# Kernel tuning notes

Measured on AMD Instinct MI355X. Metric: run time of the kernel, lower is better.

## Reference

```python
import jax, jax.numpy as jnp
import numpy as np

C = 512        # in_ch = n_heads * d_embed
NH = 8         # heads
DH = C // NH   # head dim = 64
G = 32         # groups
EPS_GN = 1e-6
EPS_LN = 1e-5


def group_norm(x, gamma, beta):
    # x: (B, C, H, W)
    B, Cc, H, W = x.shape
    xg = x.reshape(B, G, Cc // G, H, W)
    mu = xg.mean(axis=(2, 3, 4), keepdims=True)
    var = xg.var(axis=(2, 3, 4), keepdims=True)
    xg = (xg - mu) * jax.lax.rsqrt(var + EPS_GN)
    x = xg.reshape(B, Cc, H, W)
    return x * gamma[None, :, None, None] + beta[None, :, None, None]


def layer_norm(x, gamma, beta):
    mu = x.mean(axis=-1, keepdims=True)
    var = x.var(axis=-1, keepdims=True)
    return (x - mu) * jax.lax.rsqrt(var + EPS_LN) * gamma + beta


def mhsa(x, w_qkv, w_out, b_out):
    # x: (B, S, C); w_qkv: (C, 3C); w_out: (C, C)
    B, S, Cc = x.shape
    qkv = x @ w_qkv                                   # (B, S, 3C)
    q, k, v = jnp.split(qkv, 3, axis=-1)
    q = q.reshape(B, S, NH, DH).transpose(0, 2, 1, 3)  # (B, H, S, D)
    k = k.reshape(B, S, NH, DH).transpose(0, 2, 1, 3)
    v = v.reshape(B, S, NH, DH).transpose(0, 2, 1, 3)
    scores = jnp.einsum('bhsd,bhtd->bhst', q, k) / jnp.sqrt(jnp.float32(DH))
    attn = jax.nn.softmax(scores, axis=-1)
    o = jnp.einsum('bhst,bhtd->bhsd', attn, v)         # (B, H, S, D)
    o = o.transpose(0, 2, 1, 3).reshape(B, S, Cc)
    return o @ w_out + b_out


def conv1x1(x, w, b):
    # x: (B, C, H, W); w: (Cout, Cin)
    return jnp.einsum('oc,bchw->bohw', w, x) + b[None, :, None, None]


def reference(x, gn_g, gn_b, w_cin, b_cin,
              ln1_g, ln1_b, qkv1, out1_w, out1_b,
              ln2_g, ln2_b, qkv2, out2_w, out2_b,
              ln3_g, ln3_b, g1_w, g1_b, g2_w, g2_b,
              w_cout, b_cout):
    residue_long = x
    h = group_norm(x, gn_g, gn_b)
    h = conv1x1(h, w_cin, b_cin)
    B, Cc, H, W = h.shape
    h = h.reshape(B, Cc, H * W).transpose(0, 2, 1)     # (B, S, C)

    r = h
    h = mhsa(layer_norm(h, ln1_g, ln1_b), qkv1, out1_w, out1_b) + r
    r = h
    h = mhsa(layer_norm(h, ln2_g, ln2_b), qkv2, out2_w, out2_b) + r
    r = h
    g = layer_norm(h, ln3_g, ln3_b) @ g1_w + g1_b      # (B, S, 8C)
    val, gate = jnp.split(g, 2, axis=-1)
    h = (val * jax.nn.gelu(gate, approximate=False)) @ g2_w + g2_b
    h = h + r

    h = h.transpose(0, 2, 1).reshape(B, Cc, H, W)
    return conv1x1(h, w_cout, b_cout) + residue_long


def setup_inputs() -> dict:
    key = jax.random.key(0)
    ks = jax.random.split(key, 16)
    s = lambda n: 1.0 / np.sqrt(n)
    return {
        'x': jax.random.normal(ks[0], (8, C, 32, 32), jnp.float32),
        'gn_g': jnp.ones((C,), jnp.float32),
        'gn_b': jnp.zeros((C,), jnp.float32),
        'w_cin': jax.random.normal(ks[1], (C, C), jnp.float32) * s(C),
        'b_cin': jnp.zeros((C,), jnp.float32),
        'ln1_g': jnp.ones((C,), jnp.float32),
        'ln1_b': jnp.zeros((C,), jnp.float32),
        'qkv1': jax.random.normal(ks[2], (C, 3 * C), jnp.float32) * s(C),
        'out1_w': jax.random.normal(ks[3], (C, C), jnp.float32) * s(C),
        'out1_b': jnp.zeros((C,), jnp.float32),
        'ln2_g': jnp.ones((C,), jnp.float32),
        'ln2_b': jnp.zeros((C,), jnp.float32),
        'qkv2': jax.random.normal(ks[4], (C, 3 * C), jnp.float32) * s(C),
        'out2_w': jax.random.normal(ks[5], (C, C), jnp.float32) * s(C),
        'out2_b': jnp.zeros((C,), jnp.float32),
        'ln3_g': jnp.ones((C,), jnp.float32),
        'ln3_b': jnp.zeros((C,), jnp.float32),
        'g1_w': jax.random.normal(ks[6], (C, 8 * C), jnp.float32) * s(C),
        'g1_b': jnp.zeros((8 * C,), jnp.float32),
        'g2_w': jax.random.normal(ks[7], (4 * C, C), jnp.float32) * s(4 * C),
        'g2_b': jnp.zeros((C,), jnp.float32),
        'w_cout': jax.random.normal(ks[8], (C, C), jnp.float32) * s(C),
        'b_cout': jnp.zeros((C,), jnp.float32),
    }
```

## Files before the change

kernel.cpp:

```cpp
#include <hip/hip_runtime.h>
#include <hip/hip_bf16.h>
#include <math.h>

typedef __hip_bfloat16 bf16;

typedef __bf16 bf16x8 __attribute__((ext_vector_type(8)));
typedef float f32x4 __attribute__((ext_vector_type(4)));
typedef short shortx8 __attribute__((ext_vector_type(8)));

__device__ __forceinline__ float b2f_us(unsigned short u) {
    unsigned int v = ((unsigned int)u) << 16;
    return __builtin_bit_cast(float, v);
}
__device__ __forceinline__ unsigned short f2b_us(float f) {
    return __builtin_bit_cast(unsigned short, __float2bfloat16(f));
}
__device__ __forceinline__ float4 ld4(const float* p) { return *(const float4*)p; }
__device__ __forceinline__ float4 ld4(const bf16* p) {
    ushort4 u = *(const ushort4*)p;
    return make_float4(b2f_us(u.x), b2f_us(u.y), b2f_us(u.z), b2f_us(u.w));
}
__device__ __forceinline__ bf16x8 ldfrag(const bf16* p) {
    return __builtin_bit_cast(bf16x8, *(const shortx8*)p);
}
__device__ __forceinline__ f32x4 mfma16(bf16x8 a, bf16x8 b, f32x4 c) {
    return __builtin_amdgcn_mfma_f32_16x16x32_bf16(a, b, c, 0, 0, 0);
}
__device__ __forceinline__ void gload16(const bf16* g, bf16* l) {
    __builtin_amdgcn_global_load_lds(
        (const __attribute__((address_space(1))) void*)g,
        (__attribute__((address_space(3))) void*)l, 16, 0, 0);
}

struct WJob { const float* src; bf16* dst; int R, C, tile0, trans; };
struct WJobs { WJob j[8]; };

__global__ __launch_bounds__(256) void wconv_all(WJobs jobs) {
    __shared__ float tl[32][33];
    int bid = blockIdx.x;
    int ji = 0;
#pragma unroll
    for (int i = 1; i < 8; ++i)
        if (bid >= jobs.j[i].tile0) ji = i;
    WJob jb = jobs.j[ji];
    int t = bid - jb.tile0;
    int tc = jb.C >> 5;
    int tr_ = t / tc, tcx = t - tr_ * tc;
    int r0 = tr_ * 32, c0 = tcx * 32;
    const int tx = threadIdx.x & 31, ty = threadIdx.x >> 5;
    if (jb.trans) {
#pragma unroll
        for (int i = 0; i < 4; ++i)
            tl[ty + i * 8][tx] = jb.src[(long)(r0 + ty + i * 8) * jb.C + c0 + tx];
        __syncthreads();
#pragma unroll
        for (int i = 0; i < 4; ++i)
            jb.dst[(long)(c0 + ty + i * 8) * jb.R + r0 + tx] =
                __float2bfloat16(tl[tx][ty + i * 8]);
    } else {
#pragma unroll
        for (int i = 0; i < 4; ++i) {
            long idx = (long)(r0 + ty + i * 8) * jb.C + c0 + tx;
            jb.dst[idx] = __float2bfloat16(jb.src[idx]);
        }
    }
}

__global__ __launch_bounds__(256) void gn_stats_k(const float* __restrict__ x,
                                                  float* __restrict__ stats) {
    int bg = blockIdx.x;
    long base = (long)bg * 16384;
    int tid = threadIdx.x;
    float s = 0.f, sq = 0.f;
    for (int it = 0; it < 16; ++it) {
        float4 v = *(const float4*)(x + base + (long)it * 1024 + tid * 4);
        s += v.x + v.y + v.z + v.w;
        sq += v.x * v.x + v.y * v.y + v.z * v.z + v.w * v.w;
    }
#pragma unroll
    for (int off = 32; off; off >>= 1) {
        s += __shfl_down(s, off);
        sq += __shfl_down(sq, off);
    }
    __shared__ float r0[4], r1[4];
    if ((tid & 63) == 0) { r0[tid >> 6] = s; r1[tid >> 6] = sq; }
    __syncthreads();
    if (tid == 0) {
        s = r0[0] + r0[1] + r0[2] + r0[3];
        sq = r1[0] + r1[1] + r1[2] + r1[3];
        float mu = s * (1.f / 16384.f);
        float var = sq * (1.f / 16384.f) - mu * mu;
        stats[bg] = mu;
        stats[256 + bg] = rsqrtf(var + 1e-6f);
    }
}

__global__ __launch_bounds__(256) void gnxt_k(const float* __restrict__ x,
                                              const float* __restrict__ stats,
                                              const float* __restrict__ gng,
                                              const float* __restrict__ gnb,
                                              bf16* __restrict__ xt) {
    const int b = blockIdx.z;
    const int c0 = blockIdx.y * 64, s0 = blockIdx.x * 64;
    __shared__ float t[64][65];
    const int tx = threadIdx.x & 15, ty = threadIdx.x >> 4;
#pragma unroll
    for (int i = 0; i < 4; ++i) {
        int c = c0 + ty + i * 16;
        float rs = stats[256 + b * 32 + (c >> 4)];
        float ga = gng[c] * rs;
        float be = gnb[c] - stats[b * 32 + (c >> 4)] * ga;
        float4 v = *(const float4*)(x + ((long)b * 512 + c) * 1024 + s0 + tx * 4);
        t[ty + i * 16][tx * 4 + 0] = v.x * ga + be;
        t[ty + i * 16][tx * 4 + 1] = v.y * ga + be;
        t[ty + i * 16][tx * 4 + 2] = v.z * ga + be;
        t[ty + i * 16][tx * 4 + 3] = v.w * ga + be;
    }
    __syncthreads();
#pragma unroll
    for (int i = 0; i < 4; ++i) {
        int s = s0 + ty + i * 16;
        ushort4 o;
        o.x = f2b_us(t[tx * 4 + 0][ty + i * 16]);
        o.y = f2b_us(t[tx * 4 + 1][ty + i * 16]);
        o.z = f2b_us(t[tx * 4 + 2][ty + i * 16]);
        o.w = f2b_us(t[tx * 4 + 3][ty + i * 16]);
        *(ushort4*)(xt + ((long)b * 1024 + s) * 512 + c0 + tx * 4) = o;
    }
}

__global__ __launch_bounds__(256) void ln_k(const bf16* __restrict__ in,
                                            const float* __restrict__ g,
                                            const float* __restrict__ bvec,
                                            bf16* __restrict__ out) {
    long row = blockIdx.x;
    const bf16* p = in + row * 512;
    int tid = threadIdx.x;
    float v0 = b2f_us(__builtin_bit_cast(unsigned short, p[tid]));
    float v1 = b2f_us(__builtin_bit_cast(unsigned short, p[tid + 256]));
    float s = v0 + v1, sq = v0 * v0 + v1 * v1;
#pragma unroll
    for (int off = 32; off; off >>= 1) {
        s += __shfl_down(s, off);
        sq += __shfl_down(sq, off);
    }
    __shared__ float r0[4], r1[4];
    if ((tid & 63) == 0) { r0[tid >> 6] = s; r1[tid >> 6] = sq; }
    __syncthreads();
    s = r0[0] + r0[1] + r0[2] + r0[3];
    sq = r1[0] + r1[1] + r1[2] + r1[3];
    float mu = s * (1.f / 512.f);
    float var = sq * (1.f / 512.f) - mu * mu;
    float rs = rsqrtf(var + 1e-5f);
    out[row * 512 + tid] = __float2bfloat16((v0 - mu) * rs * g[tid] + bvec[tid]);
    out[row * 512 + tid + 256] =
        __float2bfloat16((v1 - mu) * rs * g[tid + 256] + bvec[tid + 256]);
}

template <bool HASBIAS, bool HASRES>
__global__ __launch_bounds__(256, 2) void mm_k(
    const bf16* __restrict__ A, const bf16* __restrict__ Bw,
    const float* __restrict__ bias, const bf16* __restrict__ res,
    bf16* __restrict__ C, int lda, int ldb, int ldc, int NT) {
    __shared__ bf16 sA[8192];
    __shared__ bf16 sB[8192];
    const int lane = threadIdx.x & 63, wave = threadIdx.x >> 6;
    const int lr = lane & 15, lg = lane >> 4;
    const int wm = wave >> 1, wn = wave & 1;
    const int m0 = blockIdx.y * 128, n0 = blockIdx.x * 128;

    f32x4 acc[4][4];
#pragma unroll
    for (int i = 0; i < 4; ++i)
#pragma unroll
        for (int j = 0; j < 4; ++j) acc[i][j] = (f32x4){0.f, 0.f, 0.f, 0.f};

    for (int t = 0; t < NT; ++t) {
        const int k0 = t * 64;
#pragma unroll
        for (int q = 0; q < 4; ++q) {
            int st = wave * 4 + q;
            int kh = st >> 3, sm = st & 7;
            gload16(A + (long)(m0 + sm * 16 + lr) * lda + k0 + kh * 32 + lg * 8,
                    &sA[st << 9]);
            gload16(Bw + (long)(n0 + sm * 16 + lr) * ldb + k0 + kh * 32 + lg * 8,
                    &sB[st << 9]);
        }
        asm volatile("s_waitcnt vmcnt(0) lgkmcnt(0)" ::: "memory");
        __builtin_amdgcn_s_barrier();
#pragma unroll
        for (int kh = 0; kh < 2; ++kh) {
            bf16x8 af[4], bfr[4];
#pragma unroll
            for (int i = 0; i < 4; ++i)
                af[i] = ldfrag(&sA[((kh * 8 + wm * 4 + i) << 9) + lane * 8]);
#pragma unroll
            for (int j = 0; j < 4; ++j)
                bfr[j] = ldfrag(&sB[((kh * 8 + wn * 4 + j) << 9) + lane * 8]);
#pragma unroll
            for (int i = 0; i < 4; ++i)
#pragma unroll
                for (int j = 0; j < 4; ++j)
                    acc[i][j] = mfma16(af[i], bfr[j], acc[i][j]);
        }
        __builtin_amdgcn_s_barrier();
    }

#pragma unroll
    for (int i = 0; i < 4; ++i) {
        int row = m0 + wm * 64 + i * 16 + lg * 4;
#pragma unroll
        for (int j = 0; j < 4; ++j) {
            int col = n0 + wn * 64 + j * 16 + lr;
            float bv = HASBIAS ? bias[col] : 0.f;
#pragma unroll
            for (int r = 0; r < 4; ++r) {
                float v = acc[i][j][r] + bv;
                if (HASRES)
                    v += b2f_us(__builtin_bit_cast(unsigned short,
                             res[(long)(row + r) * ldc + col]));
                C[(long)(row + r) * ldc + col] = __float2bfloat16(v);
            }
        }
    }
}

__global__ __launch_bounds__(256, 2) void mm_geglu_k(
    const bf16* __restrict__ A, const bf16* __restrict__ Bv,
    const bf16* __restrict__ Bg, const float* __restrict__ bias,
    bf16* __restrict__ C, int NT) {
    __shared__ bf16 sA[8192];
    __shared__ bf16 sB[8192];
    const int lane = threadIdx.x & 63, wave = threadIdx.x >> 6;
    const int lr = lane & 15, lg = lane >> 4;
    const int wm = wave >> 1, wn = wave & 1;
    const int m0 = blockIdx.y * 128, n0 = blockIdx.x * 64;

    f32x4 accv[4][2], accg[4][2];
#pragma unroll
    for (int i = 0; i < 4; ++i)
#pragma unroll
        for (int j = 0; j < 2; ++j) {
            accv[i][j] = (f32x4){0.f, 0.f, 0.f, 0.f};
            accg[i][j] = (f32x4){0.f, 0.f, 0.f, 0.f};
        }

    for (int t = 0; t < NT; ++t) {
        const int k0 = t * 64;
#pragma unroll
        for (int q = 0; q < 4; ++q) {
            int st = wave * 4 + q;
            int kh = st >> 3, sm = st & 7;
            gload16(A + (long)(m0 + sm * 16 + lr) * 512 + k0 + kh * 32 + lg * 8,
                    &sA[st << 9]);
            const bf16* bsrc = (sm < 4) ? Bv : Bg;
            int sn = sm & 3;
            gload16(bsrc + (long)(n0 + sn * 16 + lr) * 512 + k0 + kh * 32 + lg * 8,
                    &sB[st << 9]);
        }
        asm volatile("s_waitcnt vmcnt(0) lgkmcnt(0)" ::: "memory");
        __builtin_amdgcn_s_barrier();
#pragma unroll
        for (int kh = 0; kh < 2; ++kh) {
            bf16x8 af[4], bv_[2], bg_[2];
#pragma unroll
            for (int i = 0; i < 4; ++i)
                af[i] = ldfrag(&sA[((kh * 8 + wm * 4 + i) << 9) + lane * 8]);
#pragma unroll
            for (int j = 0; j < 2; ++j) {
                bv_[j] = ldfrag(&sB[((kh * 8 + wn * 2 + j) << 9) + lane * 8]);
                bg_[j] = ldfrag(&sB[((kh * 8 + 4 + wn * 2 + j) << 9) + lane * 8]);
            }
#pragma unroll
            for (int i = 0; i < 4; ++i)
#pragma unroll
                for (int j = 0; j < 2; ++j) {
                    accv[i][j] = mfma16(af[i], bv_[j], accv[i][j]);
                    accg[i][j] = mfma16(af[i], bg_[j], accg[i][j]);
                }
        }
        __builtin_amdgcn_s_barrier();
    }

#pragma unroll
    for (int i = 0; i < 4; ++i) {
        int row = m0 + wm * 64 + i * 16 + lg * 4;
#pragma unroll
        for (int j = 0; j < 2; ++j) {
            int col = n0 + (wn * 2 + j) * 16 + lr;
            float bv = bias[col], bg2 = bias[2048 + col];
#pragma unroll
            for (int r = 0; r < 4; ++r) {
                float v = accv[i][j][r] + bv;
                float g = accg[i][j][r] + bg2;
                float gl = 0.5f * g * (1.f + erff(g * 0.70710678118654752f));
                C[(long)(row + r) * 2048 + col] = __float2bfloat16(v * gl);
            }
        }
    }
}

__global__ __launch_bounds__(256) void vtrans_k(const bf16* __restrict__ qkv,
                                                bf16* __restrict__ vt) {
    const int bh = blockIdx.y;
    const int b = bh >> 3, h = bh & 7;
    const int s0 = blockIdx.x * 64;
    __shared__ bf16 tl[64][72];
    const int sl = threadIdx.x >> 2, q = threadIdx.x & 3;
    const bf16* src = qkv + ((long)b * 1024 + s0 + sl) * 1536 + 1024 + h * 64;
    *(shortx8*)&tl[sl][q * 8] = *(const shortx8*)(src + q * 8);
    *(shortx8*)&tl[sl][32 + q * 8] = *(const shortx8*)(src + 32 + q * 8);
    __syncthreads();
    const int dl = threadIdx.x >> 2;
    bf16* dst = vt + ((long)bh * 64 + dl) * 1024 + s0;
#pragma unroll
    for (int c = 0; c < 2; ++c) {
        int sb = c * 32 + q * 8;
        shortx8 o;
#pragma unroll
        for (int i = 0; i < 8; ++i)
            o[i] = __builtin_bit_cast(short, tl[sb + i][dl]);
        *(shortx8*)(dst + sb) = o;
    }
}

__global__ __launch_bounds__(256) void attn_mfma_k(const bf16* __restrict__ qkv,
                                                   const bf16* __restrict__ vt,
                                                   bf16* __restrict__ o) {
    const int wave = threadIdx.x >> 6, lane = threadIdx.x & 63;
    const int lr = lane & 15, lg = lane >> 4;
    const int h = blockIdx.y, b = blockIdx.z;
    const int q0 = blockIdx.x * 128 + wave * 32;
    __shared__ bf16 sKV[8192];
    __shared__ bf16 plds[4][16][72];
    bf16* pl = &plds[wave][0][0];
    const bf16* qbase = qkv + (long)b * 1024 * 1536 + h * 64;
    const bf16* kbase = qbase + 512;
    const bf16* vbase = vt + ((long)(b * 8 + h) * 64) * 1024;

    bf16x8 qf[2][2];
#pragma unroll
    for (int s = 0; s < 2; ++s) {
        const bf16* qp = qbase + (long)(q0 + s * 16 + lr) * 1536 + lg * 8;
#pragma unroll
        for (int c = 0; c < 2; ++c) {
            shortx8 raw = *(const shortx8*)(qp + c * 32);
            shortx8 sc;
#pragma unroll
            for (int j = 0; j < 8; ++j)
                sc[j] = __builtin_bit_cast(short,
                    f2b_us(b2f_us((unsigned short)raw[j]) * 0.125f));
            qf[s][c] = __builtin_bit_cast(bf16x8, sc);
        }
    }

    f32x4 of[2][4];
    float mrow[2][4], lrow[2][4];
#pragma unroll
    for (int s = 0; s < 2; ++s)
#pragma unroll
        for (int r = 0; r < 4; ++r) {
            of[s][r] = (f32x4){0.f, 0.f, 0.f, 0.f};
            mrow[s][r] = -1e30f;
            lrow[s][r] = 0.f;
        }

    for (int t = 0; t < 16; ++t) {
        const int kv0 = t * 64;
#pragma unroll
        for (int q = 0; q < 4; ++q) {
            int st = wave * 4 + q;
            const bf16* src;
            if (st < 8)
                src = kbase + (long)(kv0 + (st >> 1) * 16 + lr) * 1536 +
                      (st & 1) * 32 + lg * 8;
            else
                src = vbase + (long)(((st - 8) >> 1) * 16 + lr) * 1024 + kv0 +
                      (st & 1) * 32 + lg * 8;
            gload16(src, &sKV[st << 9]);
        }
        asm volatile("s_waitcnt vmcnt(0) lgkmcnt(0)" ::: "memory");
        __builtin_amdgcn_s_barrier();

        f32x4 sf[2][4];
        __builtin_amdgcn_s_setprio(1);
#pragma unroll
        for (int kt = 0; kt < 4; ++kt) {
            bf16x8 k0f = ldfrag(&sKV[(kt * 2) * 512 + lane * 8]);
            bf16x8 k1f = ldfrag(&sKV[(kt * 2 + 1) * 512 + lane * 8]);
#pragma unroll
            for (int s = 0; s < 2; ++s) {
                f32x4 z = {0.f, 0.f, 0.f, 0.f};
                z = mfma16(qf[s][0], k0f, z);
                z = mfma16(qf[s][1], k1f, z);
                sf[s][kt] = z;
            }
        }
        __builtin_amdgcn_s_setprio(0);

        bf16x8 pa[2][2];
#pragma unroll
        for (int s = 0; s < 2; ++s) {
            float mt[4];
#pragma unroll
            for (int r = 0; r < 4; ++r)
                mt[r] = fmaxf(fmaxf(sf[s][0][r], sf[s][1][r]),
                              fmaxf(sf[s][2][r], sf[s][3][r]));
#pragma unroll
            for (int m = 1; m < 16; m <<= 1)
#pragma unroll
                for (int r = 0; r < 4; ++r)
                    mt[r] = fmaxf(mt[r], __shfl_xor(mt[r], m));
            float al[4];
#pragma unroll
            for (int r = 0; r < 4; ++r) {
                float mn = fmaxf(mrow[s][r], mt[r]);
                al[r] = __expf(mrow[s][r] - mn);
                mrow[s][r] = mn;
            }
            float psum[4] = {0.f, 0.f, 0.f, 0.f};
#pragma unroll
            for (int kt = 0; kt < 4; ++kt)
#pragma unroll
                for (int r = 0; r < 4; ++r) {
                    float p = __expf(sf[s][kt][r] - mrow[s][r]);
                    psum[r] += p;
                    pl[(lg * 4 + r) * 72 + kt * 16 + lr] = __float2bfloat16(p);
                }
#pragma unroll
            for (int m = 1; m < 16; m <<= 1)
#pragma unroll
                for (int r = 0; r < 4; ++r)
                    psum[r] += __shfl_xor(psum[r], m);
#pragma unroll
            for (int r = 0; r < 4; ++r)
                lrow[s][r] = lrow[s][r] * al[r] + psum[r];
#pragma unroll
            for (int dt = 0; dt < 4; ++dt)
#pragma unroll
                for (int r = 0; r < 4; ++r) of[s][dt][r] *= al[r];
            pa[s][0] = ldfrag(pl + lr * 72 + lg * 8);
            pa[s][1] = ldfrag(pl + lr * 72 + 32 + lg * 8);
        }
        __builtin_amdgcn_s_setprio(1);
#pragma unroll
        for (int dt = 0; dt < 4; ++dt) {
            bf16x8 v0f = ldfrag(&sKV[(8 + dt * 2) * 512 + lane * 8]);
            bf16x8 v1f = ldfrag(&sKV[(8 + dt * 2 + 1) * 512 + lane * 8]);
#pragma unroll
            for (int s = 0; s < 2; ++s) {
                of[s][dt] = mfma16(pa[s][0], v0f, of[s][dt]);
                of[s][dt] = mfma16(pa[s][1], v1f, of[s][dt]);
            }
        }
        __builtin_amdgcn_s_setprio(0);
        __builtin_amdgcn_s_barrier();
    }

#pragma unroll
    for (int s = 0; s < 2; ++s) {
        bf16* op = o + ((long)b * 1024 + q0 + s * 16 + lg * 4) * 512 + h * 64 + lr;
#pragma unroll
        for (int r = 0; r < 4; ++r) {
            float inv = 1.f / lrow[s][r];
#pragma unroll
            for (int dt = 0; dt < 4; ++dt)
                op[(long)r * 512 + dt * 16] = __float2bfloat16(of[s][dt][r] * inv);
        }
    }
}

__global__ __launch_bounds__(256) void outepi_k(const bf16* __restrict__ tmp,
                                                const float* __restrict__ bcout,
                                                const float* __restrict__ x,
                                                float* __restrict__ out) {
    const int b = blockIdx.z;
    const int o0 = blockIdx.y * 64, s0 = blockIdx.x * 64;
    __shared__ float t[64][65];
    const int tx = threadIdx.x & 15, ty = threadIdx.x >> 4;
#pragma unroll
    for (int i = 0; i < 4; ++i) {
        int s = s0 + ty + i * 16;
        float4 v = ld4(tmp + ((long)b * 1024 + s) * 512 + o0 + tx * 4);
        t[ty + i * 16][tx * 4 + 0] = v.x;
        t[ty + i * 16][tx * 4 + 1] = v.y;
        t[ty + i * 16][tx * 4 + 2] = v.z;
        t[ty + i * 16][tx * 4 + 3] = v.w;
    }
    __syncthreads();
#pragma unroll
    for (int i = 0; i < 4; ++i) {
        int o = o0 + ty + i * 16;
        long idx = ((long)b * 512 + o) * 1024 + s0 + tx * 4;
        float4 xr = *(const float4*)(x + idx);
        float bc = bcout[o];
        float4 w;
        w.x = t[tx * 4 + 0][ty + i * 16] + bc + xr.x;
        w.y = t[tx * 4 + 1][ty + i * 16] + bc + xr.y;
        w.z = t[tx * 4 + 2][ty + i * 16] + bc + xr.z;
        w.w = t[tx * 4 + 3][ty + i * 16] + bc + xr.w;
        *(float4*)(out + idx) = w;
    }
}

extern "C" void kernel_launch(void* const* d_in, const int* in_sizes, int n_in,
                              void* d_out, int out_size, void* d_ws, size_t ws_size,
                              hipStream_t stream) {
    const float* x = (const float*)d_in[0];
    const float* gn_g = (const float*)d_in[1];
    const float* gn_b = (const float*)d_in[2];
    const float* w_cin = (const float*)d_in[3];
    const float* b_cin = (const float*)d_in[4];
    const float* ln1_g = (const float*)d_in[5];
    const float* ln1_b = (const float*)d_in[6];
    const float* qkv1w = (const float*)d_in[7];
    const float* out1_w = (const float*)d_in[8];
    const float* out1_b = (const float*)d_in[9];
    const float* ln2_g = (const float*)d_in[10];
    const float* ln2_b = (const float*)d_in[11];
    const float* qkv2w = (const float*)d_in[12];
    const float* out2_w = (const float*)d_in[13];
    const float* out2_b = (const float*)d_in[14];
    const float* ln3_g = (const float*)d_in[15];
    const float* ln3_b = (const float*)d_in[16];
    const float* g1_w = (const float*)d_in[17];
    const float* g1_b = (const float*)d_in[18];
    const float* g2_w = (const float*)d_in[19];
    const float* g2_b = (const float*)d_in[20];
    const float* w_cout = (const float*)d_in[21];
    const float* b_cout = (const float*)d_in[22];
    float* out = (float*)d_out;

    char* ws = (char*)d_ws;
    float* stats = (float*)ws;
    bf16* wq1 = (bf16*)(ws + 4096);
    bf16* wo1 = wq1 + 1536 * 512;
    bf16* wq2 = wo1 + 512 * 512;
    bf16* wo2 = wq2 + 1536 * 512;
    bf16* wg1 = wo2 + 512 * 512;
    bf16* wg2 = wg1 + 4096 * 512;
    bf16* wci = wg2 + 512 * 2048;
    bf16* wco = wci + 512 * 512;
    bf16* h = wco + 512 * 512;
    bf16* h2 = h + (size_t)8192 * 512;
    bf16* lnb = h2 + (size_t)8192 * 512;
    bf16* qkv = lnb + (size_t)8192 * 512;
    bf16* obuf = qkv + (size_t)8192 * 1536;
    bf16* gg = qkv;
    bf16* vt = lnb;

    WJobs jobs;
    jobs.j[0] = {qkv1w, wq1, 512, 1536, 0, 1};
    jobs.j[1] = {out1_w, wo1, 512, 512, 768, 1};
    jobs.j[2] = {qkv2w, wq2, 512, 1536, 1024, 1};
    jobs.j[3] = {out2_w, wo2, 512, 512, 1792, 1};
    jobs.j[4] = {g1_w, wg1, 512, 4096, 2048, 1};
    jobs.j[5] = {g2_w, wg2, 2048, 512, 4096, 1};
    jobs.j[6] = {w_cin, wci, 512, 512, 5120, 0};
    jobs.j[7] = {w_cout, wco, 512, 512, 5376, 0};
    wconv_all<<<5632, 256, 0, stream>>>(jobs);

    gn_stats_k<<<256, 256, 0, stream>>>(x, stats);
    gnxt_k<<<dim3(16, 8, 8), 256, 0, stream>>>(x, stats, gn_g, gn_b, lnb);
    mm_k<true, false><<<dim3(4, 64), 256, 0, stream>>>(
        lnb, wci, b_cin, nullptr, h, 512, 512, 512, 8);

    ln_k<<<8192, 256, 0, stream>>>(h, ln1_g, ln1_b, lnb);
    mm_k<false, false><<<dim3(12, 64), 256, 0, stream>>>(
        lnb, wq1, nullptr, nullptr, qkv, 512, 512, 1536, 8);
    vtrans_k<<<dim3(16, 64), 256, 0, stream>>>(qkv, vt);
    attn_mfma_k<<<dim3(8, 8, 8), 256, 0, stream>>>(qkv, vt, obuf);
    mm_k<true, true><<<dim3(4, 64), 256, 0, stream>>>(
        obuf, wo1, out1_b, h, h2, 512, 512, 512, 8);

    ln_k<<<8192, 256, 0, stream>>>(h2, ln2_g, ln2_b, lnb);
    mm_k<false, false><<<dim3(12, 64), 256, 0, stream>>>(
        lnb, wq2, nullptr, nullptr, qkv, 512, 512, 1536, 8);
    vtrans_k<<<dim3(16, 64), 256, 0, stream>>>(qkv, vt);
    attn_mfma_k<<<dim3(8, 8, 8), 256, 0, stream>>>(qkv, vt, obuf);
    mm_k<true, true><<<dim3(4, 64), 256, 0, stream>>>(
        obuf, wo2, out2_b, h2, h, 512, 512, 512, 8);

    ln_k<<<8192, 256, 0, stream>>>(h, ln3_g, ln3_b, lnb);
    mm_geglu_k<<<dim3(32, 64), 256, 0, stream>>>(
        lnb, wg1, wg1 + (size_t)2048 * 512, g1_b, gg, 8);
    mm_k<true, true><<<dim3(4, 64), 256, 0, stream>>>(
        gg, wg2, g2_b, h, h2, 2048, 2048, 512, 32);

    mm_k<false, false><<<dim3(4, 64), 256, 0, stream>>>(
        h2, wco, nullptr, nullptr, lnb, 512, 512, 512, 8);
    outepi_k<<<dim3(16, 8, 8), 256, 0, stream>>>(lnb, b_cout, x, out);
}
```

Measured before the change: 436.2 us.

## Double-buffer LDS tiles in GEMM and attention kernels, narrow N=512 GEMM tiles

Adds LDS double buffering to the GEMM, GEGLU GEMM and flash-attention kernels, so the next K/V or K-tile is fetched with direct-to-LDS loads while the current tile feeds the MFMAs. The goal is to hide global-load latency that previously sat between loads and compute. Separately, N=512 GEMMs switch to 128x64 tiles, doubling the grid from 256 to 512 blocks to fill more CUs. LDS use doubles, which may lower occupancy, most likely in the attention kernel.

New measurement: 439.2 us. About the same (+0.7%).

```diff
diff --git a/kernel.cpp b/kernel.cpp
--- a/kernel.cpp
+++ b/kernel.cpp
@@ -157,52 +157,79 @@
         __float2bfloat16((v1 - mu) * rs * g[tid + 256] + bvec[tid + 256]);
 }
 
-template <bool HASBIAS, bool HASRES>
+template <bool HASBIAS, bool HASRES, int BN>
 __global__ __launch_bounds__(256, 2) void mm_k(
     const bf16* __restrict__ A, const bf16* __restrict__ Bw,
     const float* __restrict__ bias, const bf16* __restrict__ res,
     bf16* __restrict__ C, int lda, int ldb, int ldc, int NT) {
-    __shared__ bf16 sA[8192];
-    __shared__ bf16 sB[8192];
+    constexpr int NJ = BN / 64 * 2;
+    __shared__ bf16 sA[2][8192];
+    __shared__ bf16 sB[2][BN == 128 ? 8192 : 4096];
     const int lane = threadIdx.x & 63, wave = threadIdx.x >> 6;
     const int lr = lane & 15, lg = lane >> 4;
     const int wm = wave >> 1, wn = wave & 1;
-    const int m0 = blockIdx.y * 128, n0 = blockIdx.x * 128;
-
-    f32x4 acc[4][4];
+    const int m0 = blockIdx.y * 128, n0 = blockIdx.x * BN;
+
+    f32x4 acc[4][NJ];
 #pragma unroll
     for (int i = 0; i < 4; ++i)
 #pragma unroll
-        for (int j = 0; j < 4; ++j) acc[i][j] = (f32x4){0.f, 0.f, 0.f, 0.f};
-
-    for (int t = 0; t < NT; ++t) {
-        const int k0 = t * 64;
+        for (int j = 0; j < NJ; ++j) acc[i][j] = (f32x4){0.f, 0.f, 0.f, 0.f};
+
+    auto stage = [&](int buf, int k0) {
 #pragma unroll
         for (int q = 0; q < 4; ++q) {
             int st = wave * 4 + q;
             int kh = st >> 3, sm = st & 7;
             gload16(A + (long)(m0 + sm * 16 + lr) * lda + k0 + kh * 32 + lg * 8,
-                    &sA[st << 9]);
-            gload16(Bw + (long)(n0 + sm * 16 + lr) * ldb + k0 + kh * 32 + lg * 8,
-                    &sB[st << 9]);
-        }
-        asm volatile("s_waitcnt vmcnt(0) lgkmcnt(0)" ::: "memory");
-        __builtin_amdgcn_s_barrier();
+                    &sA[buf][st << 9]);
+        }
+        if (BN == 128) {
+#pragma unroll
+            for (int q = 0; q < 4; ++q) {
+                int st = wave * 4 + q;
+                int kh = st >> 3, sn = st & 7;
+                gload16(Bw + (long)(n0 + sn * 16 + lr) * ldb + k0 + kh * 32 + lg * 8,
+                        &sB[buf][st << 9]);
+            }
+        } else {
+#pragma unroll
+            for (int q = 0; q < 2; ++q) {
+                int bs = wave * 2 + q;
+                int kh = bs >> 2, sn = bs & 3;
+                gload16(Bw + (long)(n0 + sn * 16 + lr) * ldb + k0 + kh * 32 + lg * 8,
+                        &sB[buf][bs << 9]);
+            }
+        }
+    };
+    auto compute = [&](int buf) {
 #pragma unroll
         for (int kh = 0; kh < 2; ++kh) {
-            bf16x8 af[4], bfr[4];
+            bf16x8 af[4], bfr[NJ];
 #pragma unroll
             for (int i = 0; i < 4; ++i)
-                af[i] = ldfrag(&sA[((kh * 8 + wm * 4 + i) << 9) + lane * 8]);
-#pragma unroll
-            for (int j = 0; j < 4; ++j)
-                bfr[j] = ldfrag(&sB[((kh * 8 + wn * 4 + j) << 9) + lane * 8]);
+                af[i] = ldfrag(&sA[buf][((kh * 8 + wm * 4 + i) << 9) + lane * 8]);
+#pragma unroll
+            for (int j = 0; j < NJ; ++j) {
+                int bs = BN == 128 ? (kh * 8 + wn * 4 + j) : (kh * 4 + wn * 2 + j);
+                bfr[j] = ldfrag(&sB[buf][(bs << 9) + lane * 8]);
+            }
 #pragma unroll
             for (int i = 0; i < 4; ++i)
 #pragma unroll
-                for (int j = 0; j < 4; ++j)
+                for (int j = 0; j < NJ; ++j)
                     acc[i][j] = mfma16(af[i], bfr[j], acc[i][j]);
         }
+    };
+
+    stage(0, 0);
+    asm volatile("s_waitcnt vmcnt(0)" ::: "memory");
+    __builtin_amdgcn_s_barrier();
+    for (int t = 0; t < NT; ++t) {
+        if (t + 1 < NT) stage((t + 1) & 1, (t + 1) * 64);
+        __builtin_amdgcn_sched_barrier(0);
+        compute(t & 1);
+        asm volatile("s_waitcnt vmcnt(0)" ::: "memory");
         __builtin_amdgcn_s_barrier();
     }
 
@@ -210,8 +237,8 @@
     for (int i = 0; i < 4; ++i) {
         int row = m0 + wm * 64 + i * 16 + lg * 4;
 #pragma unroll
-        for (int j = 0; j < 4; ++j) {
-            int col = n0 + wn * 64 + j * 16 + lr;
+        for (int j = 0; j < NJ; ++j) {
+            int col = n0 + wn * (BN / 2) + j * 16 + lr;
             float bv = HASBIAS ? bias[col] : 0.f;
 #pragma unroll
             for (int r = 0; r < 4; ++r) {
@@ -229,8 +256,8 @@
     const bf16* __restrict__ A, const bf16* __restrict__ Bv,
     const bf16* __restrict__ Bg, const float* __restrict__ bias,
     bf16* __restrict__ C, int NT) {
-    __shared__ bf16 sA[8192];
-    __shared__ bf16 sB[8192];
+    __shared__ bf16 sA[2][8192];
+    __shared__ bf16 sB[2][8192];
     const int lane = threadIdx.x & 63, wave = threadIdx.x >> 6;
     const int lr = lane & 15, lg = lane >> 4;
     const int wm = wave >> 1, wn = wave & 1;
@@ -245,31 +272,30 @@
             accg[i][j] = (f32x4){0.f, 0.f, 0.f, 0.f};
         }
 
-    for (int t = 0; t < NT; ++t) {
-        const int k0 = t * 64;
+    auto stage = [&](int buf, int k0) {
 #pragma unroll
         for (int q = 0; q < 4; ++q) {
             int st = wave * 4 + q;
             int kh = st >> 3, sm = st & 7;
             gload16(A + (long)(m0 + sm * 16 + lr) * 512 + k0 + kh * 32 + lg * 8,
-                    &sA[st << 9]);
+                    &sA[buf][st << 9]);
             const bf16* bsrc = (sm < 4) ? Bv : Bg;
             int sn = sm & 3;
             gload16(bsrc + (long)(n0 + sn * 16 + lr) * 512 + k0 + kh * 32 + lg * 8,
-                    &sB[st << 9]);
-        }
-        asm volatile("s_waitcnt vmcnt(0) lgkmcnt(0)" ::: "memory");
-        __builtin_amdgcn_s_barrier();
+                    &sB[buf][st << 9]);
+        }
+    };
+    auto compute = [&](int buf) {
 #pragma unroll
         for (int kh = 0; kh < 2; ++kh) {
             bf16x8 af[4], bv_[2], bg_[2];
 #pragma unroll
             for (int i = 0; i < 4; ++i)
-                af[i] = ldfrag(&sA[((kh * 8 + wm * 4 + i) << 9) + lane * 8]);
+                af[i] = ldfrag(&sA[buf][((kh * 8 + wm * 4 + i) << 9) + lane * 8]);
 #pragma unroll
             for (int j = 0; j < 2; ++j) {
-                bv_[j] = ldfrag(&sB[((kh * 8 + wn * 2 + j) << 9) + lane * 8]);
-                bg_[j] = ldfrag(&sB[((kh * 8 + 4 + wn * 2 + j) << 9) + lane * 8]);
+                bv_[j] = ldfrag(&sB[buf][((kh * 8 + wn * 2 + j) << 9) + lane * 8]);
+                bg_[j] = ldfrag(&sB[buf][((kh * 8 + 4 + wn * 2 + j) << 9) + lane * 8]);
             }
 #pragma unroll
             for (int i = 0; i < 4; ++i)
@@ -279,6 +305,16 @@
                     accg[i][j] = mfma16(af[i], bg_[j], accg[i][j]);
                 }
         }
+    };
+
+    stage(0, 0);
+    asm volatile("s_waitcnt vmcnt(0)" ::: "memory");
+    __builtin_amdgcn_s_barrier();
+    for (int t = 0; t < NT; ++t) {
+        if (t + 1 < NT) stage((t + 1) & 1, (t + 1) * 64);
+        __builtin_amdgcn_sched_barrier(0);
+        compute(t & 1);
+        asm volatile("s_waitcnt vmcnt(0)" ::: "memory");
         __builtin_amdgcn_s_barrier();
     }
 
@@ -331,7 +367,7 @@
     const int lr = lane & 15, lg = lane >> 4;
     const int h = blockIdx.y, b = blockIdx.z;
     const int q0 = blockIdx.x * 128 + wave * 32;
-    __shared__ bf16 sKV[8192];
+    __shared__ bf16 sKV[2][8192];
     __shared__ bf16 plds[4][16][72];
     bf16* pl = &plds[wave][0][0];
     const bf16* qbase = qkv + (long)b * 1024 * 1536 + h * 64;
@@ -365,8 +401,7 @@
             lrow[s][r] = 0.f;
         }
 
-    for (int t = 0; t < 16; ++t) {
-        const int kv0 = t * 64;
+    auto stageKV = [&](int buf, int kv0) {
 #pragma unroll
         for (int q = 0; q < 4; ++q) {
             int st = wave * 4 + q;
@@ -377,17 +412,17 @@
             else
                 src = vbase + (long)(((st - 8) >> 1) * 16 + lr) * 1024 + kv0 +
                       (st & 1) * 32 + lg * 8;
-            gload16(src, &sKV[st << 9]);
-        }
-        asm volatile("s_waitcnt vmcnt(0) lgkmcnt(0)" ::: "memory");
-        __builtin_amdgcn_s_barrier();
-
+            gload16(src, &sKV[buf][st << 9]);
+        }
+    };
+    auto computeKV = [&](int buf) {
+        const bf16* base = &sKV[buf][0];
         f32x4 sf[2][4];
         __builtin_amdgcn_s_setprio(1);
 #pragma unroll
         for (int kt = 0; kt < 4; ++kt) {
-            bf16x8 k0f = ldfrag(&sKV[(kt * 2) * 512 + lane * 8]);
-            bf16x8 k1f = ldfrag(&sKV[(kt * 2 + 1) * 512 + lane * 8]);
+            bf16x8 k0f = ldfrag(base + (kt * 2) * 512 + lane * 8);
+            bf16x8 k1f = ldfrag(base + (kt * 2 + 1) * 512 + lane * 8);
 #pragma unroll
             for (int s = 0; s < 2; ++s) {
                 f32x4 z = {0.f, 0.f, 0.f, 0.f};
@@ -445,8 +480,8 @@
         __builtin_amdgcn_s_setprio(1);
 #pragma unroll
         for (int dt = 0; dt < 4; ++dt) {
-            bf16x8 v0f = ldfrag(&sKV[(8 + dt * 2) * 512 + lane * 8]);
-            bf16x8 v1f = ldfrag(&sKV[(8 + dt * 2 + 1) * 512 + lane * 8]);
+            bf16x8 v0f = ldfrag(base + (8 + dt * 2) * 512 + lane * 8);
+            bf16x8 v1f = ldfrag(base + (8 + dt * 2 + 1) * 512 + lane * 8);
 #pragma unroll
             for (int s = 0; s < 2; ++s) {
                 of[s][dt] = mfma16(pa[s][0], v0f, of[s][dt]);
@@ -454,6 +489,16 @@
             }
         }
         __builtin_amdgcn_s_setprio(0);
+    };
+
+    stageKV(0, 0);
+    asm volatile("s_waitcnt vmcnt(0)" ::: "memory");
+    __builtin_amdgcn_s_barrier();
+    for (int t = 0; t < 16; ++t) {
+        if (t < 15) stageKV((t + 1) & 1, (t + 1) * 64);
+        __builtin_amdgcn_sched_barrier(0);
+        computeKV(t & 1);
+        asm volatile("s_waitcnt vmcnt(0)" ::: "memory");
         __builtin_amdgcn_s_barrier();
     }
 
@@ -562,32 +607,32 @@
 
     gn_stats_k<<<256, 256, 0, stream>>>(x, stats);
     gnxt_k<<<dim3(16, 8, 8), 256, 0, stream>>>(x, stats, gn_g, gn_b, lnb);
-    mm_k<true, false><<<dim3(4, 64), 256, 0, stream>>>(
+    mm_k<true, false, 64><<<dim3(8, 64), 256, 0, stream>>>(
         lnb, wci, b_cin, nullptr, h, 512, 512, 512, 8);
 
     ln_k<<<8192, 256, 0, stream>>>(h, ln1_g, ln1_b, lnb);
-    mm_k<false, false><<<dim3(12, 64), 256, 0, stream>>>(
+    mm_k<false, false, 128><<<dim3(12, 64), 256, 0, stream>>>(
         lnb, wq1, nullptr, nullptr, qkv, 512, 512, 1536, 8);
     vtrans_k<<<dim3(16, 64), 256, 0, stream>>>(qkv, vt);
     attn_mfma_k<<<dim3(8, 8, 8), 256, 0, stream>>>(qkv, vt, obuf);
-    mm_k<true, true><<<dim3(4, 64), 256, 0, stream>>>(
+    mm_k<true, true, 64><<<dim3(8, 64), 256, 0, stream>>>(
         obuf, wo1, out1_b, h, h2, 512, 512, 512, 8);
 
     ln_k<<<8192, 256, 0, stream>>>(h2, ln2_g, ln2_b, lnb);
-    mm_k<false, false><<<dim3(12, 64), 256, 0, stream>>>(
+    mm_k<false, false, 128><<<dim3(12, 64), 256, 0, stream>>>(
         lnb, wq2, nullptr, nullptr, qkv, 512, 512, 1536, 8);
     vtrans_k<<<dim3(16, 64), 256, 0, stream>>>(qkv, vt);
     attn_mfma_k<<<dim3(8, 8, 8), 256, 0, stream>>>(qkv, vt, obuf);
-    mm_k<true, true><<<dim3(4, 64), 256, 0, stream>>>(
+    mm_k<true, true, 64><<<dim3(8, 64), 256, 0, stream>>>(
         obuf, wo2, out2_b, h2, h, 512, 512, 512, 8);
 
     ln_k<<<8192, 256, 0, stream>>>(h, ln3_g, ln3_b, lnb);
     mm_geglu_k<<<dim3(32, 64), 256, 0, stream>>>(
         lnb, wg1, wg1 + (size_t)2048 * 512, g1_b, gg, 8);
-    mm_k<true, true><<<dim3(4, 64), 256, 0, stream>>>(
+    mm_k<true, true, 64><<<dim3(8, 64), 256, 0, stream>>>(
         gg, wg2, g2_b, h, h2, 2048, 2048, 512, 32);
 
-    mm_k<false, false><<<dim3(4, 64), 256, 0, stream>>>(
+    mm_k<false, false, 64><<<dim3(8, 64), 256, 0, stream>>>(
         h2, wco, nullptr, nullptr, lnb, 512, 512, 512, 8);
     outepi_k<<<dim3(16, 8, 8), 256, 0, stream>>>(lnb, b_cout, x, out);
 }
```
